# Performance work log

Measured on AMD Instinct MI355X. Metric: run time of the kernel, lower is better.

Reference implementation:

```python
import jax, jax.numpy as jnp
import numpy as np

P_MIN = 0.8        # minimum cumulative probability mass kept per row
THRESHOLD = 1e-10  # drop matches with probability below this
EPS = 1e-6         # distance clamp (matches dist.clamp(min=1e-6) in backward)

B, N, M, D = 4, 4096, 4096, 3


def setup_inputs() -> dict:
    key = jax.random.key(0)
    kx, ky = jax.random.split(key)
    x = jax.random.normal(kx, (B, N, D), dtype=jnp.float32)
    y = jax.random.normal(ky, (B, M, D), dtype=jnp.float32)
    return {"x": x, "y": y}


def _pairwise_dist(x, y):
    # ||x_i - y_j|| via Gram trick; avoids materializing [B,N,M,D] diff tensor.
    sq = (
        jnp.sum(x * x, axis=-1)[:, :, None]
        + jnp.sum(y * y, axis=-1)[:, None, :]
        - 2.0 * jnp.einsum("bnd,bmd->bnm", x, y)
    )
    return jnp.sqrt(jnp.maximum(sq, EPS * EPS))  # [B, N, M]


def _sparse_match_weights(d):
    # Row-wise soft matching probabilities over targets j.
    p = jax.nn.softmax(-d, axis=-1)  # [B, N, M]
    # Keep the most-probable entries per row until cumulative mass reaches P_MIN
    # (the dense, jit-friendly equivalent of the COO compaction in the kernel).
    order = jnp.argsort(-p, axis=-1)
    p_sorted = jnp.take_along_axis(p, order, axis=-1)
    csum = jnp.cumsum(p_sorted, axis=-1)
    keep_sorted = (csum - p_sorted) < P_MIN  # include entry that crosses P_MIN
    inv = jnp.argsort(order, axis=-1)
    keep = jnp.take_along_axis(keep_sorted, inv, axis=-1)
    return jnp.where(keep & (p > THRESHOLD), p, 0.0)  # sparse COO values, dense layout


def reference(x, y):
    d = _pairwise_dist(x, y)                     # [B, N, M]
    w = jax.lax.stop_gradient(_sparse_match_weights(d))  # weights are constants in bwd
    loss = jnp.sum(w * d)                        # scalar matching loss
    return loss
```

## Files before the change

kernel.cpp:

```cpp
#include <hip/hip_runtime.h>


#define MCOLS 4096
#define KPT   64
#define WPB   8
#define P_MIN 0.8f

template <int CTRL, int RM, int BM, bool BC>
__device__ __forceinline__ float dpp_mov0(float x) {
    return __int_as_float(__builtin_amdgcn_update_dpp(
        0, __float_as_int(x), CTRL, RM, BM, BC));
}
__device__ __forceinline__ float dppSum(float v) {
    v += dpp_mov0<0x111, 0xF, 0xF, true >(v);
    v += dpp_mov0<0x112, 0xF, 0xF, true >(v);
    v += dpp_mov0<0x114, 0xF, 0xF, true >(v);
    v += dpp_mov0<0x118, 0xF, 0xF, true >(v);
    v += dpp_mov0<0x142, 0xA, 0xF, false>(v);
    v += dpp_mov0<0x143, 0xC, 0xF, false>(v);
    return __int_as_float(__builtin_amdgcn_readlane(__float_as_int(v), 63));
}
__device__ __forceinline__ void dppSum2(float& a, float& b) {
    a += dpp_mov0<0x111, 0xF, 0xF, true >(a); b += dpp_mov0<0x111, 0xF, 0xF, true >(b);
    a += dpp_mov0<0x112, 0xF, 0xF, true >(a); b += dpp_mov0<0x112, 0xF, 0xF, true >(b);
    a += dpp_mov0<0x114, 0xF, 0xF, true >(a); b += dpp_mov0<0x114, 0xF, 0xF, true >(b);
    a += dpp_mov0<0x118, 0xF, 0xF, true >(a); b += dpp_mov0<0x118, 0xF, 0xF, true >(b);
    a += dpp_mov0<0x142, 0xA, 0xF, false>(a); b += dpp_mov0<0x142, 0xA, 0xF, false>(b);
    a += dpp_mov0<0x143, 0xC, 0xF, false>(a); b += dpp_mov0<0x143, 0xC, 0xF, false>(b);
    a = __int_as_float(__builtin_amdgcn_readlane(__float_as_int(a), 63));
    b = __int_as_float(__builtin_amdgcn_readlane(__float_as_int(b), 63));
}
__device__ __forceinline__ float dppMax(float v) {
    v = fmaxf(v, dpp_mov0<0x111, 0xF, 0xF, true >(v));
    v = fmaxf(v, dpp_mov0<0x112, 0xF, 0xF, true >(v));
    v = fmaxf(v, dpp_mov0<0x114, 0xF, 0xF, true >(v));
    v = fmaxf(v, dpp_mov0<0x118, 0xF, 0xF, true >(v));
    v = fmaxf(v, dpp_mov0<0x142, 0xA, 0xF, false>(v));
    v = fmaxf(v, dpp_mov0<0x143, 0xC, 0xF, false>(v));
    return __int_as_float(__builtin_amdgcn_readlane(__float_as_int(v), 63));
}

__global__ __launch_bounds__(WPB * 64) void apml_row_wave(
        const float* __restrict__ x, const float* __restrict__ y,
        float* __restrict__ partial, float* __restrict__ out) {
    __shared__ __align__(16) float scomp[WPB * 256];

    const int tid  = threadIdx.x;
    const int wid  = tid >> 6;
    const int lane = tid & 63;
    const int row  = blockIdx.x * WPB + wid;
    const int b    = row >> 12;

    const float x0 = x[row * 3 + 0];
    const float x1 = x[row * 3 + 1];
    const float x2 = x[row * 3 + 2];
    const float* yb = y + (size_t)b * MCOLS * 3;

    float p[KPT];
    float zl = 0.0f;
    #pragma unroll
    for (int k = 0; k < KPT; ++k) {
        const int j = k * 64 + lane;
        const float y0 = yb[j * 3 + 0];
        const float y1 = yb[j * 3 + 1];
        const float y2 = yb[j * 3 + 2];
        const float dx = x0 - y0, dy = x1 - y1, dz = x2 - y2;
        const float sq = fmaxf(dx * dx + dy * dy + dz * dz, 1e-12f);
        const float pk = __expf(-sqrtf(sq));
        p[k] = pk;
        zl  += pk;
    }
    const float Z      = dppSum(zl);
    const float target = P_MIN * Z;
    const float pTop   = 1.0f;

    float ssl = 0.0f, ssh = pTop;
    {
        float eGl = 16.0f * dppSum(p[0] + p[1] + p[2] + p[3]);
        float eGh = 0.0f;
        for (int it = 0; it < 5; ++it) {
            float s;
            if (it & 1) {
                s = 0.5f * (ssl + ssh);
            } else {
                const float den = fmaxf(eGl - eGh, 1e-30f);
                s = ssl + (ssh - ssl) * ((eGl - target) / den);
            }
            if (!(s > ssl && s < ssh)) s = 0.5f * (ssl + ssh);
            if (!(s > ssl && s < ssh)) break;
            float m = 0.0f;
            #pragma unroll
            for (int q = 0; q < 4; ++q) m += (p[q] >= s) ? p[q] : 0.0f;
            m = 16.0f * dppSum(m);
            if (m >= target) { ssl = s; eGl = m; }
            else             { ssh = s; eGh = m; }
        }
    }

    float sl = 0.0f, sh = pTop;
    float Gl = Z,    Gh = 0.0f;
    int   Cl = MCOLS, Ch = 0;
    {
        float ml = 0.0f, mh = 0.0f;
        int   cl_ = 0,   ch_ = 0;
        #pragma unroll
        for (int k = 0; k < KPT; ++k) {
            const float pk = p[k];
            const bool gl = (pk >= ssl);
            const bool gh = (pk >= ssh);
            ml += gl ? pk : 0.0f; cl_ += (int)__popcll(__ballot(gl));
            mh += gh ? pk : 0.0f; ch_ += (int)__popcll(__ballot(gh));
        }
        dppSum2(ml, mh);
        if (ml >= target) { sl = ssl; Gl = ml; Cl = cl_; }
        else              { sh = ssl; Gh = ml; Ch = cl_; }
        if (mh >= target) { sl = ssh; Gl = mh; Cl = ch_; }
        else if (ssh < sh){ sh = ssh; Gh = mh; Ch = ch_; }
    }

    for (int it = 0; it < 10 && (Cl - Ch) > 256; ++it) {
        float s;
        if (it & 1) {
            s = 0.5f * (sl + sh);
        } else {
            const float den = fmaxf(Gl - Gh, 1e-30f);
            s = sl + (sh - sl) * ((Gl - target) / den);
        }
        if (!(s > sl && s < sh)) s = 0.5f * (sl + sh);
        if (!(s > sl && s < sh)) break;

        float m0 = 0.0f, m1 = 0.0f, m2 = 0.0f, m3 = 0.0f;
        int   c = 0;
        #pragma unroll
        for (int k = 0; k < KPT; k += 4) {
            const bool g0 = (p[k]     >= s);
            const bool g1 = (p[k + 1] >= s);
            const bool g2 = (p[k + 2] >= s);
            const bool g3 = (p[k + 3] >= s);
            m0 += g0 ? p[k]     : 0.0f; c += (int)__popcll(__ballot(g0));
            m1 += g1 ? p[k + 1] : 0.0f; c += (int)__popcll(__ballot(g1));
            m2 += g2 ? p[k + 2] : 0.0f; c += (int)__popcll(__ballot(g2));
            m3 += g3 ? p[k + 3] : 0.0f; c += (int)__popcll(__ballot(g3));
        }
        const float m = dppSum((m0 + m1) + (m2 + m3));
        if (m >= target) { sl = s; Gl = m; Cl = c; }
        else             { sh = s; Gh = m; Ch = c; }
    }

    int C = 0;
    #pragma unroll
    for (int k = 0; k < KPT; ++k) {
        const bool band = (p[k] >= sl) && (p[k] < sh);
        const unsigned long long mk = __ballot(band);
        if (band) {
            const unsigned mlo = (unsigned)mk, mhi = (unsigned)(mk >> 32);
            const int within = __builtin_amdgcn_mbcnt_hi(
                                   mhi, __builtin_amdgcn_mbcnt_lo(mlo, 0));
            const int pos = C + within;
            if (pos < 256) scomp[wid * 256 + pos] = p[k];
        }
        C += (int)__popcll(mk);
    }
    __builtin_amdgcn_s_waitcnt(0);
    float cp[4];
    bool  cv[4];
    #pragma unroll
    for (int q = 0; q < 4; ++q) {
        const int idx = q * 64 + lane;
        cv[q] = (idx < C) && (idx < 256);
        cp[q] = cv[q] ? scomp[wid * 256 + idx] : 0.0f;
    }

    float pstar, mb = 0.0f;
    int   cnt = 1;
    bool  haveTie;

    if (C > 256) {
        pstar = (sl > 0.0f) ? __uint_as_float(__float_as_uint(sl) - 1u) : 0.0f;
        haveTie = false;
    } else {
        float lo_s = sl, hi_s = sh, lo_G = Gl, hi_G = Gh;
        int   lo_C = Cl, hi_C = Ch;
        for (int it = 0; it < 10 && (lo_C - hi_C) > 2; ++it) {
            float s;
            if (it & 1) {
                s = 0.5f * (lo_s + hi_s);
            } else {
                const float den = fmaxf(lo_G - hi_G, 1e-30f);
                s = lo_s + (hi_s - lo_s) * ((lo_G - target) / den);
            }
            if (!(s > lo_s && s < hi_s)) s = 0.5f * (lo_s + hi_s);
            if (!(s > lo_s && s < hi_s)) break;

            float m = 0.0f;
            int   c = Ch;
            #pragma unroll
            for (int q = 0; q < 4; ++q) {
                const bool ge = cv[q] && (cp[q] >= s);
                m += ge ? cp[q] : 0.0f;
                c += (int)__popcll(__ballot(ge));
            }
            m = Gh + dppSum(m);
            if (m >= target) { lo_s = s; lo_G = m; lo_C = c; }
            else             { hi_s = s; hi_G = m; hi_C = c; }
        }

        float scur = hi_s, M = hi_G;
        bool ok = false;
        pstar = lo_s;
        for (int e = 0; e < 16; ++e) {
            float vl = 0.0f;
            #pragma unroll
            for (int q = 0; q < 4; ++q)
                vl = fmaxf(vl, (cv[q] && cp[q] < scur) ? cp[q] : 0.0f);
            const float v = dppMax(vl);
            if (!(v > 0.0f)) break;
            int cvn = 0;
            #pragma unroll
            for (int q = 0; q < 4; ++q)
                cvn += (int)__popcll(__ballot(cv[q] && (cp[q] == v)));
            const float Mn = M + v * (float)cvn;
            if (Mn >= target) { pstar = v; mb = M; cnt = cvn; ok = true; break; }
            M = Mn; scur = v;
        }
        haveTie = ok;
        if (!ok) {
            pstar = (lo_s > 0.0f) ? __uint_as_float(__float_as_uint(lo_s) - 1u)
                                  : 0.0f;
        }
    }

    float spd = 0.0f;
    #pragma unroll
    for (int k = 0; k < KPT; ++k) {
        const float t = (p[k] > pstar) ? p[k] : 1.0f;
        spd += t * (-__logf(t));
    }
    spd = dppSum(spd);

    if (lane == 0) {
        float tie = 0.0f;
        if (haveTie) {
            const float R = (target - mb) / pstar;
            int q = (int)ceilf(R);
            if (q < 1) q = 1;
            if (q > cnt) q = cnt;
            tie = (float)q * pstar * (-__logf(pstar));
        }
        const float v = (spd + tie) / Z;
        if (partial) partial[row] = v;
        else         atomicAdd(out, v);
    }
}

__global__ __launch_bounds__(1024) void apml_reduce(
        const float* __restrict__ partial, float* __restrict__ out, int n) {
    __shared__ float s[16];
    const int t = threadIdx.x;
    float a = 0.0f;
    #pragma unroll
    for (int q = 0; q < 16; ++q) {
        const int i = t * 16 + q;
        a += (i < n) ? partial[i] : 0.0f;
    }
    a = dppSum(a);
    if ((t & 63) == 0) s[t >> 6] = a;
    __syncthreads();
    if (t == 0) {
        float r = 0.0f;
        #pragma unroll
        for (int w = 0; w < 16; ++w) r += s[w];
        out[0] = r;
    }
}

extern "C" void kernel_launch(void* const* d_in, const int* in_sizes, int n_in,
                              void* d_out, int out_size, void* d_ws, size_t ws_size,
                              hipStream_t stream) {
    const float* x = (const float*)d_in[0];
    const float* y = (const float*)d_in[1];
    float* out = (float*)d_out;

    const int nrows = in_sizes[0] / 3;
    const int nblocks = nrows / WPB;

    const size_t part_bytes = (size_t)nrows * sizeof(float);

    if (d_ws && ws_size >= part_bytes && nrows <= 16384) {
        float* partial = (float*)d_ws;
        apml_row_wave<<<nblocks, WPB * 64, 0, stream>>>(x, y, partial, out);
        apml_reduce<<<1, 1024, 0, stream>>>(partial, out, nrows);
    } else {
        hipMemsetAsync(out, 0, sizeof(float), stream);
        apml_row_wave<<<nblocks, WPB * 64, 0, stream>>>(x, y, nullptr, out);
    }
}
```

Baseline: 183.9 us.

## Move per-row probabilities from registers to LDS with one wave per block

Each row's 4096 probabilities now live in shared memory instead of a 64-entry register array. Each block is a single 64-thread wave, and the register-heavy loops are only partially unrolled. The aim is to cut VGPR pressure and raise occupancy. In exchange, every threshold pass re-reads LDS, and each wave now uses 17KB of LDS, which itself caps occupancy. The search upper bound also changes from 1.0 to just above the row max.

```diff
diff --git a/kernel.cpp b/kernel.cpp
--- a/kernel.cpp
+++ b/kernel.cpp
@@ -3,7 +3,6 @@
 
 #define MCOLS 4096
 #define KPT   64
-#define WPB   8
 #define P_MIN 0.8f
 
 template <int CTRL, int RM, int BM, bool BC>
@@ -40,15 +39,14 @@
     return __int_as_float(__builtin_amdgcn_readlane(__float_as_int(v), 63));
 }
 
-__global__ __launch_bounds__(WPB * 64) void apml_row_wave(
+__global__ __launch_bounds__(64) void apml_row_lds(
         const float* __restrict__ x, const float* __restrict__ y,
         float* __restrict__ partial, float* __restrict__ out) {
-    __shared__ __align__(16) float scomp[WPB * 256];
-
-    const int tid  = threadIdx.x;
-    const int wid  = tid >> 6;
-    const int lane = tid & 63;
-    const int row  = blockIdx.x * WPB + wid;
+    __shared__ __align__(16) float pl[KPT * 64];
+    __shared__ __align__(16) float scomp[256];
+
+    const int lane = threadIdx.x;
+    const int row  = blockIdx.x;
     const int b    = row >> 12;
 
     const float x0 = x[row * 3 + 0];
@@ -56,9 +54,8 @@
     const float x2 = x[row * 3 + 2];
     const float* yb = y + (size_t)b * MCOLS * 3;
 
-    float p[KPT];
-    float zl = 0.0f;
-    #pragma unroll
+    float zl = 0.0f, pml = 0.0f;
+    #pragma unroll 4
     for (int k = 0; k < KPT; ++k) {
         const int j = k * 64 + lane;
         const float y0 = yb[j * 3 + 0];
@@ -67,16 +64,21 @@
         const float dx = x0 - y0, dy = x1 - y1, dz = x2 - y2;
         const float sq = fmaxf(dx * dx + dy * dy + dz * dz, 1e-12f);
         const float pk = __expf(-sqrtf(sq));
-        p[k] = pk;
+        pl[j] = pk;
         zl  += pk;
-    }
-    const float Z      = dppSum(zl);
+        pml  = fmaxf(pml, pk);
+    }
+    __builtin_amdgcn_s_waitcnt(0);
+    const float Z    = dppSum(zl);
+    const float pmax = dppMax(pml);
     const float target = P_MIN * Z;
-    const float pTop   = 1.0f;
-
+    const float pTop = __uint_as_float(__float_as_uint(pmax) + 1u);
+
+    const float q0 = pl[lane], q1 = pl[64 + lane];
+    const float q2 = pl[128 + lane], q3 = pl[192 + lane];
     float ssl = 0.0f, ssh = pTop;
     {
-        float eGl = 16.0f * dppSum(p[0] + p[1] + p[2] + p[3]);
+        float eGl = 16.0f * dppSum(q0 + q1 + q2 + q3);
         float eGh = 0.0f;
         for (int it = 0; it < 5; ++it) {
             float s;
@@ -88,9 +90,10 @@
             }
             if (!(s > ssl && s < ssh)) s = 0.5f * (ssl + ssh);
             if (!(s > ssl && s < ssh)) break;
-            float m = 0.0f;
-            #pragma unroll
-            for (int q = 0; q < 4; ++q) m += (p[q] >= s) ? p[q] : 0.0f;
+            float m = (q0 >= s) ? q0 : 0.0f;
+            m += (q1 >= s) ? q1 : 0.0f;
+            m += (q2 >= s) ? q2 : 0.0f;
+            m += (q3 >= s) ? q3 : 0.0f;
             m = 16.0f * dppSum(m);
             if (m >= target) { ssl = s; eGl = m; }
             else             { ssh = s; eGh = m; }
@@ -103,9 +106,9 @@
     {
         float ml = 0.0f, mh = 0.0f;
         int   cl_ = 0,   ch_ = 0;
-        #pragma unroll
+        #pragma unroll 4
         for (int k = 0; k < KPT; ++k) {
-            const float pk = p[k];
+            const float pk = pl[k * 64 + lane];
             const bool gl = (pk >= ssl);
             const bool gh = (pk >= ssh);
             ml += gl ? pk : 0.0f; cl_ += (int)__popcll(__ballot(gl));
@@ -131,16 +134,17 @@
 
         float m0 = 0.0f, m1 = 0.0f, m2 = 0.0f, m3 = 0.0f;
         int   c = 0;
-        #pragma unroll
         for (int k = 0; k < KPT; k += 4) {
-            const bool g0 = (p[k]     >= s);
-            const bool g1 = (p[k + 1] >= s);
-            const bool g2 = (p[k + 2] >= s);
-            const bool g3 = (p[k + 3] >= s);
-            m0 += g0 ? p[k]     : 0.0f; c += (int)__popcll(__ballot(g0));
-            m1 += g1 ? p[k + 1] : 0.0f; c += (int)__popcll(__ballot(g1));
-            m2 += g2 ? p[k + 2] : 0.0f; c += (int)__popcll(__ballot(g2));
-            m3 += g3 ? p[k + 3] : 0.0f; c += (int)__popcll(__ballot(g3));
+            const float p0 = pl[(k    ) * 64 + lane];
+            const float p1 = pl[(k + 1) * 64 + lane];
+            const float p2 = pl[(k + 2) * 64 + lane];
+            const float p3 = pl[(k + 3) * 64 + lane];
+            const bool g0 = (p0 >= s), g1 = (p1 >= s);
+            const bool g2 = (p2 >= s), g3 = (p3 >= s);
+            m0 += g0 ? p0 : 0.0f; c += (int)__popcll(__ballot(g0));
+            m1 += g1 ? p1 : 0.0f; c += (int)__popcll(__ballot(g1));
+            m2 += g2 ? p2 : 0.0f; c += (int)__popcll(__ballot(g2));
+            m3 += g3 ? p3 : 0.0f; c += (int)__popcll(__ballot(g3));
         }
         const float m = dppSum((m0 + m1) + (m2 + m3));
         if (m >= target) { sl = s; Gl = m; Cl = c; }
@@ -148,16 +152,17 @@
     }
 
     int C = 0;
-    #pragma unroll
+    #pragma unroll 2
     for (int k = 0; k < KPT; ++k) {
-        const bool band = (p[k] >= sl) && (p[k] < sh);
+        const float pk = pl[k * 64 + lane];
+        const bool band = (pk >= sl) && (pk < sh);
         const unsigned long long mk = __ballot(band);
         if (band) {
             const unsigned mlo = (unsigned)mk, mhi = (unsigned)(mk >> 32);
             const int within = __builtin_amdgcn_mbcnt_hi(
                                    mhi, __builtin_amdgcn_mbcnt_lo(mlo, 0));
             const int pos = C + within;
-            if (pos < 256) scomp[wid * 256 + pos] = p[k];
+            if (pos < 256) scomp[pos] = pk;
         }
         C += (int)__popcll(mk);
     }
@@ -168,7 +173,7 @@
     for (int q = 0; q < 4; ++q) {
         const int idx = q * 64 + lane;
         cv[q] = (idx < C) && (idx < 256);
-        cp[q] = cv[q] ? scomp[wid * 256 + idx] : 0.0f;
+        cp[q] = cv[q] ? scomp[idx] : 0.0f;
     }
 
     float pstar, mb = 0.0f;
@@ -230,13 +235,22 @@
         }
     }
 
-    float spd = 0.0f;
-    #pragma unroll
-    for (int k = 0; k < KPT; ++k) {
-        const float t = (p[k] > pstar) ? p[k] : 1.0f;
-        spd += t * (-__logf(t));
-    }
-    spd = dppSum(spd);
+    float s0 = 0.0f, s1 = 0.0f, s2 = 0.0f, s3 = 0.0f;
+    for (int k = 0; k < KPT; k += 4) {
+        const float p0 = pl[(k    ) * 64 + lane];
+        const float p1 = pl[(k + 1) * 64 + lane];
+        const float p2 = pl[(k + 2) * 64 + lane];
+        const float p3 = pl[(k + 3) * 64 + lane];
+        const float t0 = (p0 > pstar) ? p0 : 1.0f;
+        const float t1 = (p1 > pstar) ? p1 : 1.0f;
+        const float t2 = (p2 > pstar) ? p2 : 1.0f;
+        const float t3 = (p3 > pstar) ? p3 : 1.0f;
+        s0 += t0 * (-__logf(t0));
+        s1 += t1 * (-__logf(t1));
+        s2 += t2 * (-__logf(t2));
+        s3 += t3 * (-__logf(t3));
+    }
+    const float spd = dppSum((s0 + s1) + (s2 + s3));
 
     if (lane == 0) {
         float tie = 0.0f;
@@ -282,16 +296,14 @@
     float* out = (float*)d_out;
 
     const int nrows = in_sizes[0] / 3;
-    const int nblocks = nrows / WPB;
-
     const size_t part_bytes = (size_t)nrows * sizeof(float);
 
     if (d_ws && ws_size >= part_bytes && nrows <= 16384) {
         float* partial = (float*)d_ws;
-        apml_row_wave<<<nblocks, WPB * 64, 0, stream>>>(x, y, partial, out);
+        apml_row_lds<<<nrows, 64, 0, stream>>>(x, y, partial, out);
         apml_reduce<<<1, 1024, 0, stream>>>(partial, out, nrows);
     } else {
         hipMemsetAsync(out, 0, sizeof(float), stream);
-        apml_row_wave<<<nblocks, WPB * 64, 0, stream>>>(x, y, nullptr, out);
-    }
-}
+        apml_row_lds<<<nrows, 64, 0, stream>>>(x, y, nullptr, out);
+    }
+}
```

Result: slower. 255.4 us (+38.9%).
